# Kernel optimization log

Hardware: AMD Instinct MI355X
Metric: run time of the kernel (lower is better)

## Reference

```python
import jax, jax.numpy as jnp
import numpy as np

B, N, D = 8, 2048, 512  # batch, input_dim (tokens), weight_dim


def setup_inputs() -> dict:
    key = jax.random.key(0)
    ks = jax.random.split(key, 7)
    return {
        "query": jax.random.normal(ks[0], (B, N, D), dtype=jnp.float32),
        "key": jax.random.normal(ks[1], (B, N, D), dtype=jnp.float32),
        "value": jax.random.normal(ks[2], (B, N, D), dtype=jnp.float32),
        "W_query": jax.random.normal(ks[3], (D, D), dtype=jnp.float32),
        "W_key": jax.random.normal(ks[4], (D, D), dtype=jnp.float32),
        "W_value": jax.random.normal(ks[5], (D, D), dtype=jnp.float32),
        "self_importance": jnp.zeros((N,), dtype=jnp.float32),
    }


def reference(query, key, value, W_query, W_key, W_value, self_importance):
    d = W_query.shape[0]
    q = jnp.einsum("bnd,de->bne", query, W_query)
    k = jnp.einsum("bnd,de->bne", key, W_key)
    v = jnp.einsum("bnd,de->bne", value, W_value)
    scores = jnp.einsum("bqe,bke->bqk", q, k) / jnp.sqrt(jnp.float32(d))
    # diagonal self-importance bias: eye(N) * clamp(exp(s), max=3)
    importance = jnp.minimum(jnp.exp(self_importance), 3.0)  # [N]
    n = scores.shape[1]
    idx = jnp.arange(n)
    scores = scores.at[:, idx, idx].add(importance)
    attn = jax.nn.softmax(scores, axis=-1)  # [B, N, N]
    entropy_loss = -jnp.mean(jnp.sum(attn * jnp.log(attn + 1e-10), axis=-1))
    out = jnp.einsum("bqk,bke->bqe", attn, v)
    return (out, attn, entropy_loss)
```

## Files before the change

### kernel.cpp

```cpp
#include <hip/hip_runtime.h>
#include <math.h>

#define BB 8
#define NN 2048
#define DD 512

typedef _Float16 half8 __attribute__((ext_vector_type(8)));
typedef _Float16 half4 __attribute__((ext_vector_type(4)));
typedef float f32x4 __attribute__((ext_vector_type(4)));

#define GLOAD16(gp, sp) __builtin_amdgcn_global_load_lds( \
    (const __attribute__((address_space(1))) void*)(gp), \
    (__attribute__((address_space(3))) void*)(sp), 16, 0, 0)

__global__ __launch_bounds__(256) void wsplit_kernel(
    const float* __restrict__ Wq, const float* __restrict__ Wk, const float* __restrict__ Wv,
    _Float16* __restrict__ qhT, _Float16* __restrict__ qlT,
    _Float16* __restrict__ khT, _Float16* __restrict__ klT,
    _Float16* __restrict__ vhT)
{
    __shared__ float t[64][65];
    const int z = blockIdx.z;
    const float* W = (z == 0) ? Wq : ((z == 1) ? Wk : Wv);
    _Float16* Ph = (z == 0) ? qhT : ((z == 1) ? khT : vhT);
    _Float16* Pl = (z == 0) ? qlT : ((z == 1) ? klT : nullptr);
    const int bx = blockIdx.x * 64, by = blockIdx.y * 64;
    const int tid = threadIdx.x;
    #pragma unroll
    for (int i = 0; i < 16; ++i) {
        const int idx = i * 256 + tid;
        const int r = idx >> 6, c = idx & 63;
        t[r][c] = W[(long)(by + r) * 512 + bx + c];
    }
    __syncthreads();
    #pragma unroll
    for (int i = 0; i < 16; ++i) {
        const int idx = i * 256 + tid;
        const int r = idx >> 6, c = idx & 63;
        const float v = t[c][r];
        const _Float16 h = (_Float16)v;
        const long o = (long)(bx + r) * 512 + by + c;
        Ph[o] = h;
        if (z < 2) Pl[o] = (_Float16)(v - (float)h);
    }
}

template<int EPI>
__global__ __launch_bounds__(256) void mm_nt(
    const float* __restrict__ Af,
    const _Float16* __restrict__ Agh, const _Float16* __restrict__ Agl,
    const _Float16* __restrict__ Bgh, const _Float16* __restrict__ Bgl,
    float* __restrict__ Of, _Float16* __restrict__ Oh, _Float16* __restrict__ Ol,
    const float* __restrict__ si,
    int N, int K, long sAb, long sBb, long sOb, float scale)
{
    constexpr bool NP3    = (EPI == 0 || EPI == 2);
    constexpr bool A_FP32 = (EPI == 0 || EPI == 1);
    constexpr bool A_SPLIT = (EPI == 0);

    __shared__ __align__(16) _Float16 smem[(NP3 ? 4 : 2) * 128 * 32];
    _Float16* Ah = smem;
    _Float16* Bh = smem + 4096;
    _Float16* Al = smem + 8192;
    _Float16* Bl = smem + 12288;

    const int tid  = threadIdx.x;
    const int lane = tid & 63;
    const int w    = tid >> 6;
    const int wr   = w >> 1, wc = w & 1;
    const int z    = blockIdx.z;
    const int bm   = blockIdx.y * 128, bn = blockIdx.x * 128;

    const float* Afz = nullptr;
    const _Float16 *Aghz = nullptr, *Aglz = nullptr;
    if constexpr (A_FP32) { Afz = Af + (long)z * sAb; }
    else { Aghz = Agh + (long)z * sAb; if constexpr (NP3) Aglz = Agl + (long)z * sAb; }
    const _Float16* Bghz = Bgh + (long)z * sBb;
    const _Float16* Bglz = nullptr;
    if constexpr (NP3) Bglz = Bgl + (long)z * sBb;

    f32x4 acc[4][4];
    #pragma unroll
    for (int i = 0; i < 4; ++i)
        #pragma unroll
        for (int j = 0; j < 4; ++j) acc[i][j] = (f32x4)0.0f;

    for (int k0 = 0; k0 < K; k0 += 32) {
        #pragma unroll
        for (int i = 0; i < 2; ++i) {
            const int c   = i * 256 + w * 64 + lane;
            const int row = c >> 2, sl = c & 3;
            const long g  = (long)(bn + row) * K + k0 + sl * 8;
            const int lb  = (i * 256 + w * 64) * 8;
            GLOAD16(Bghz + g, Bh + lb);
            if constexpr (NP3) GLOAD16(Bglz + g, Bl + lb);
        }
        if constexpr (A_FP32) {
            #pragma unroll
            for (int i = 0; i < 4; ++i) {
                const int c = tid + i * 256;
                const int row = c >> 3, q4 = c & 7;
                const float4 v = *(const float4*)(Afz + (long)(bm + row) * K + k0 + q4 * 4);
                half4 h;
                h[0] = (_Float16)v.x; h[1] = (_Float16)v.y;
                h[2] = (_Float16)v.z; h[3] = (_Float16)v.w;
                *(half4*)&Ah[row * 32 + q4 * 4] = h;
                if constexpr (A_SPLIT) {
                    half4 l;
                    l[0] = (_Float16)(v.x - (float)h[0]);
                    l[1] = (_Float16)(v.y - (float)h[1]);
                    l[2] = (_Float16)(v.z - (float)h[2]);
                    l[3] = (_Float16)(v.w - (float)h[3]);
                    *(half4*)&Al[row * 32 + q4 * 4] = l;
                }
            }
        } else {
            #pragma unroll
            for (int i = 0; i < 2; ++i) {
                const int c   = i * 256 + w * 64 + lane;
                const int row = c >> 2, sl = c & 3;
                const long g  = (long)(bm + row) * K + k0 + sl * 8;
                const int lb  = (i * 256 + w * 64) * 8;
                GLOAD16(Aghz + g, Ah + lb);
                if constexpr (NP3) GLOAD16(Aglz + g, Al + lb);
            }
        }
        __syncthreads();

        half8 ah[4], bh[4], al[4], bl[4];
        #pragma unroll
        for (int f = 0; f < 4; ++f) {
            const int ar = wr * 64 + f * 16 + (lane & 15);
            const int ao = ar * 32 + ((lane >> 4) << 3);
            ah[f] = *(const half8*)&Ah[ao];
            if constexpr (NP3) al[f] = *(const half8*)&Al[ao];
            const int br = wc * 64 + f * 16 + (lane & 15);
            const int bo = br * 32 + ((lane >> 4) << 3);
            bh[f] = *(const half8*)&Bh[bo];
            if constexpr (NP3) bl[f] = *(const half8*)&Bl[bo];
        }
        #pragma unroll
        for (int i = 0; i < 4; ++i)
            #pragma unroll
            for (int j = 0; j < 4; ++j) {
                acc[i][j] = __builtin_amdgcn_mfma_f32_16x16x32_f16(ah[i], bh[j], acc[i][j], 0, 0, 0);
                if constexpr (NP3) {
                    acc[i][j] = __builtin_amdgcn_mfma_f32_16x16x32_f16(ah[i], bl[j], acc[i][j], 0, 0, 0);
                    acc[i][j] = __builtin_amdgcn_mfma_f32_16x16x32_f16(al[i], bh[j], acc[i][j], 0, 0, 0);
                }
            }
        __syncthreads();
    }

    #pragma unroll
    for (int i = 0; i < 4; ++i) {
        const int rb = bm + wr * 64 + i * 16 + ((lane >> 4) << 2);
        #pragma unroll
        for (int j = 0; j < 4; ++j) {
            const int gc = bn + wc * 64 + j * 16 + (lane & 15);
            if constexpr (EPI == 0) {
                #pragma unroll
                for (int r = 0; r < 4; ++r) {
                    const float vv = acc[i][j][r];
                    const _Float16 h = (_Float16)vv;
                    const long o = (long)(rb + r) * N + gc;
                    Oh[o] = h;
                    Ol[o] = (_Float16)(vv - (float)h);
                }
            } else if constexpr (EPI == 1) {
                half4 hv;
                #pragma unroll
                for (int r = 0; r < 4; ++r) hv[r] = (_Float16)acc[i][j][r];
                const int b = rb >> 11, rIn = rb & 2047;
                *(half4*)&Oh[((long)b * 512 + gc) * 2048 + rIn] = hv;
            } else if constexpr (EPI == 2) {
                float* O = Of + (long)z * sOb;
                #pragma unroll
                for (int r = 0; r < 4; ++r) {
                    const int gr = rb + r;
                    float vv = acc[i][j][r] * scale;
                    if (gr == gc) vv += fminf(expf(si[gr]), 3.0f);
                    O[(long)gr * N + gc] = vv;
                }
            } else {
                float* O = Of + (long)z * sOb;
                #pragma unroll
                for (int r = 0; r < 4; ++r)
                    O[(long)(rb + r) * N + gc] = acc[i][j][r];
            }
        }
    }
}

__global__ __launch_bounds__(256) void softmax_entropy_kernel(
    float* __restrict__ attn, _Float16* __restrict__ ah, float* __restrict__ partials)
{
    __shared__ float red[4];
    const long row = blockIdx.x;
    float* p = attn + row * (long)NN;
    _Float16* ph = ah + row * (long)NN;
    const int tid = threadIdx.x;
    const int base = tid * 8;

    float4 va = *(const float4*)(p + base);
    float4 vb = *(const float4*)(p + base + 4);
    float v[8] = {va.x, va.y, va.z, va.w, vb.x, vb.y, vb.z, vb.w};

    float m = v[0];
    #pragma unroll
    for (int i = 1; i < 8; ++i) m = fmaxf(m, v[i]);
    #pragma unroll
    for (int o = 32; o; o >>= 1) m = fmaxf(m, __shfl_xor(m, o, 64));
    if ((tid & 63) == 0) red[tid >> 6] = m;
    __syncthreads();
    m = fmaxf(fmaxf(red[0], red[1]), fmaxf(red[2], red[3]));

    float t[8];
    float s = 0.f;
    #pragma unroll
    for (int i = 0; i < 8; ++i) { t[i] = v[i] - m; v[i] = expf(t[i]); s += v[i]; }
    #pragma unroll
    for (int o = 32; o; o >>= 1) s += __shfl_xor(s, o, 64);
    __syncthreads();
    if ((tid & 63) == 0) red[tid >> 6] = s;
    __syncthreads();
    s = red[0] + red[1] + red[2] + red[3];

    const float inv = 1.0f / s;
    const float lns = logf(s);
    float e = 0.f;
    float pv[8];
    #pragma unroll
    for (int i = 0; i < 8; ++i) {
        pv[i] = v[i] * inv;
        e = fmaf(pv[i], t[i] - lns, e);
    }
    *(float4*)(p + base)     = make_float4(pv[0], pv[1], pv[2], pv[3]);
    *(float4*)(p + base + 4) = make_float4(pv[4], pv[5], pv[6], pv[7]);
    half8 h;
    #pragma unroll
    for (int i = 0; i < 8; ++i) h[i] = (_Float16)pv[i];
    *(half8*)(ph + base) = h;

    #pragma unroll
    for (int o = 32; o; o >>= 1) e += __shfl_xor(e, o, 64);
    __syncthreads();
    if ((tid & 63) == 0) red[tid >> 6] = e;
    __syncthreads();
    if (tid == 0) partials[row] = red[0] + red[1] + red[2] + red[3];
}

__global__ __launch_bounds__(256) void ent_reduce_kernel(
    const float* __restrict__ partials, float* __restrict__ ent)
{
    __shared__ float red[4];
    float s = 0.f;
    for (int i = threadIdx.x; i < BB * NN; i += 256) s += partials[i];
    #pragma unroll
    for (int o = 32; o; o >>= 1) s += __shfl_xor(s, o, 64);
    if ((threadIdx.x & 63) == 0) red[threadIdx.x >> 6] = s;
    __syncthreads();
    if (threadIdx.x == 0)
        *ent = -(red[0] + red[1] + red[2] + red[3]) / (float)(BB * NN);
}

extern "C" void kernel_launch(void* const* d_in, const int* in_sizes, int n_in,
                              void* d_out, int out_size, void* d_ws, size_t ws_size,
                              hipStream_t stream) {
    const float* query = (const float*)d_in[0];
    const float* key   = (const float*)d_in[1];
    const float* value = (const float*)d_in[2];
    const float* Wq    = (const float*)d_in[3];
    const float* Wk    = (const float*)d_in[4];
    const float* Wv    = (const float*)d_in[5];
    const float* si    = (const float*)d_in[6];

    float* out  = (float*)d_out;
    float* attn = out + (size_t)BB * NN * DD;
    float* ent  = attn + (size_t)BB * NN * NN;

    const size_t NK = (size_t)BB * NN * DD;
    _Float16* ws16 = (_Float16*)d_ws;
    _Float16* qh = ws16;
    _Float16* ql = qh + NK;
    _Float16* kh = ql + NK;
    _Float16* kl = kh + NK;
    _Float16* vT = kl + NK;
    _Float16* WqhT = vT + NK;
    _Float16* WqlT = WqhT + DD * DD;
    _Float16* WkhT = WqlT + DD * DD;
    _Float16* WklT = WkhT + DD * DD;
    _Float16* WvhT = WklT + DD * DD;
    float* partials = (float*)(WvhT + DD * DD);
    _Float16* attn_h = ws16;

    const dim3 blk(256);
    const float inv_sqrt_d = 0.044194173824159216f;

    wsplit_kernel<<<dim3(8, 8, 3), blk, 0, stream>>>(Wq, Wk, Wv,
        WqhT, WqlT, WkhT, WklT, WvhT);

    mm_nt<0><<<dim3(4, 128, 1), blk, 0, stream>>>(
        query, nullptr, nullptr, WqhT, WqlT, nullptr, qh, ql, nullptr,
        DD, DD, 0, 0, 0, 1.0f);
    mm_nt<0><<<dim3(4, 128, 1), blk, 0, stream>>>(
        key, nullptr, nullptr, WkhT, WklT, nullptr, kh, kl, nullptr,
        DD, DD, 0, 0, 0, 1.0f);
    mm_nt<1><<<dim3(4, 128, 1), blk, 0, stream>>>(
        value, nullptr, nullptr, WvhT, nullptr, nullptr, vT, nullptr, nullptr,
        DD, DD, 0, 0, 0, 1.0f);

    mm_nt<2><<<dim3(16, 16, BB), blk, 0, stream>>>(
        nullptr, qh, ql, kh, kl, attn, nullptr, nullptr, si,
        NN, DD, (long)NN * DD, (long)NN * DD, (long)NN * NN, inv_sqrt_d);

    softmax_entropy_kernel<<<dim3(BB * NN), blk, 0, stream>>>(attn, attn_h, partials);
    ent_reduce_kernel<<<dim3(1), blk, 0, stream>>>(partials, ent);

    mm_nt<3><<<dim3(4, 16, BB), blk, 0, stream>>>(
        nullptr, attn_h, nullptr, vT, nullptr, out, nullptr, nullptr, nullptr,
        DD, NN, (long)NN * NN, (long)DD * NN, (long)NN * DD, 1.0f);
}
```

Baseline: 348.5 us.

## Replace scores GEMM with 256x256-tile double-buffered split-fp16 MFMA kernel

The QK^T scores GEMM moves from the generic 128x128 mm_nt kernel to a dedicated 512-thread kernel with 256x256 output tiles. It uses a register-staged double-buffered LDS pipeline with an XOR swizzle, MFMA priority hints, and a remapped block order for L2 locality. The goal is more data reuse per tile and overlap of global loads with MFMA work in the three-product hi/lo fp16 compensation GEMM. The cost is 128KB of dynamic LDS and a large accumulator footprint per thread, which limits occupancy and risks register spills.

```diff
diff --git a/kernel.cpp b/kernel.cpp
--- a/kernel.cpp
+++ b/kernel.cpp
@@ -5,6 +5,7 @@
 #define NN 2048
 #define DD 512
 
+typedef _Float16 halfT;
 typedef _Float16 half8 __attribute__((ext_vector_type(8)));
 typedef _Float16 half4 __attribute__((ext_vector_type(4)));
 typedef float f32x4 __attribute__((ext_vector_type(4)));
@@ -54,7 +55,7 @@
     const float* __restrict__ si,
     int N, int K, long sAb, long sBb, long sOb, float scale)
 {
-    constexpr bool NP3    = (EPI == 0 || EPI == 2);
+    constexpr bool NP3    = (EPI == 0);
     constexpr bool A_FP32 = (EPI == 0 || EPI == 1);
     constexpr bool A_SPLIT = (EPI == 0);
 
@@ -122,7 +123,6 @@
                 const long g  = (long)(bm + row) * K + k0 + sl * 8;
                 const int lb  = (i * 256 + w * 64) * 8;
                 GLOAD16(Aghz + g, Ah + lb);
-                if constexpr (NP3) GLOAD16(Aglz + g, Al + lb);
             }
         }
         __syncthreads();
@@ -173,20 +173,151 @@
                 for (int r = 0; r < 4; ++r) hv[r] = (_Float16)acc[i][j][r];
                 const int b = rb >> 11, rIn = rb & 2047;
                 *(half4*)&Oh[((long)b * 512 + gc) * 2048 + rIn] = hv;
-            } else if constexpr (EPI == 2) {
-                float* O = Of + (long)z * sOb;
-                #pragma unroll
-                for (int r = 0; r < 4; ++r) {
-                    const int gr = rb + r;
-                    float vv = acc[i][j][r] * scale;
-                    if (gr == gc) vv += fminf(expf(si[gr]), 3.0f);
-                    O[(long)gr * N + gc] = vv;
-                }
             } else {
                 float* O = Of + (long)z * sOb;
                 #pragma unroll
                 for (int r = 0; r < 4; ++r)
                     O[(long)(rb + r) * N + gc] = acc[i][j][r];
+            }
+        }
+    }
+}
+
+__global__ __launch_bounds__(512, 2) void scores256_kernel(
+    const halfT* __restrict__ qh, const halfT* __restrict__ ql,
+    const halfT* __restrict__ kh, const halfT* __restrict__ kl,
+    float* __restrict__ C, const float* __restrict__ si, float scale)
+{
+    extern __shared__ __align__(16) char smem[];
+
+    const int tid  = threadIdx.x;
+    const int lane = tid & 63;
+    const int w    = tid >> 6;
+    const int wr   = w >> 2, wc = w & 3;
+
+    int flat = (blockIdx.z << 6) | (blockIdx.y << 3) | blockIdx.x;
+    flat = ((flat & 7) << 6) | (flat >> 3);
+    const int bx = flat & 7, by = (flat >> 3) & 7, bz = flat >> 6;
+    const int bm = by * 256, bn = bx * 256;
+
+    const long zoff = (long)bz * NN * DD;
+    const halfT* A_h = qh + zoff;
+    const halfT* A_l = ql + zoff;
+    const halfT* B_h = kh + zoff;
+    const halfT* B_l = kl + zoff;
+
+    const int s_row0 = tid >> 2, s_sl = tid & 3;
+    const int s_row1 = s_row0 + 128;
+    const int s_off0 = s_row0 * 64 + ((s_sl ^ (s_row0 & 3)) << 4);
+    const int s_off1 = s_row1 * 64 + ((s_sl ^ (s_row1 & 3)) << 4);
+    const long gA0 = (long)(bm + s_row0) * DD + s_sl * 8;
+    const long gA1 = (long)(bm + s_row1) * DD + s_sl * 8;
+    const long gB0 = (long)(bn + s_row0) * DD + s_sl * 8;
+    const long gB1 = (long)(bn + s_row1) * DD + s_sl * 8;
+
+    const int q = lane >> 4;
+    const int frag_off = (lane & 15) * 64 + ((q ^ (lane & 3)) << 4);
+    const int aoff = wr * 8192 + frag_off;
+    const int boff = wc * 4096 + frag_off;
+
+    f32x4 acc[8][4];
+    #pragma unroll
+    for (int m = 0; m < 8; ++m)
+        #pragma unroll
+        for (int n = 0; n < 4; ++n) acc[m][n] = (f32x4)0.0f;
+
+    float4 sreg[8];
+    auto load_tile = [&](int t) {
+        const long kk = (long)t * 32;
+        sreg[0] = *(const float4*)(A_h + gA0 + kk);
+        sreg[1] = *(const float4*)(A_h + gA1 + kk);
+        sreg[2] = *(const float4*)(A_l + gA0 + kk);
+        sreg[3] = *(const float4*)(A_l + gA1 + kk);
+        sreg[4] = *(const float4*)(B_h + gB0 + kk);
+        sreg[5] = *(const float4*)(B_h + gB1 + kk);
+        sreg[6] = *(const float4*)(B_l + gB0 + kk);
+        sreg[7] = *(const float4*)(B_l + gB1 + kk);
+    };
+    auto write_tile = [&](char* setp) {
+        *(float4*)(setp +     0 + s_off0) = sreg[0];
+        *(float4*)(setp +     0 + s_off1) = sreg[1];
+        *(float4*)(setp + 16384 + s_off0) = sreg[2];
+        *(float4*)(setp + 16384 + s_off1) = sreg[3];
+        *(float4*)(setp + 32768 + s_off0) = sreg[4];
+        *(float4*)(setp + 32768 + s_off1) = sreg[5];
+        *(float4*)(setp + 49152 + s_off0) = sreg[6];
+        *(float4*)(setp + 49152 + s_off1) = sreg[7];
+    };
+
+    load_tile(0);
+    write_tile(smem);
+    load_tile(1);
+    asm volatile("s_waitcnt lgkmcnt(0)" ::: "memory");
+    __builtin_amdgcn_s_barrier();
+    __builtin_amdgcn_sched_barrier(0);
+
+    for (int t = 0; t < 16; ++t) {
+        char* cur = smem + (size_t)(t & 1) * 65536;
+        char* nxt = smem + (size_t)((t + 1) & 1) * 65536;
+
+        if (t < 15) write_tile(nxt);
+        if (t < 14) load_tile(t + 2);
+        __builtin_amdgcn_sched_barrier(0);
+
+        half8 ah[8], bh[4], bl[4];
+        #pragma unroll
+        for (int n = 0; n < 4; ++n)
+            bh[n] = *(const half8*)(cur + 32768 + boff + n * 1024);
+        #pragma unroll
+        for (int m = 0; m < 8; ++m)
+            ah[m] = *(const half8*)(cur +     0 + aoff + m * 1024);
+        __builtin_amdgcn_s_setprio(1);
+        #pragma unroll
+        for (int m = 0; m < 8; ++m)
+            #pragma unroll
+            for (int n = 0; n < 4; ++n)
+                acc[m][n] = __builtin_amdgcn_mfma_f32_16x16x32_f16(ah[m], bh[n], acc[m][n], 0, 0, 0);
+        __builtin_amdgcn_s_setprio(0);
+        #pragma unroll
+        for (int n = 0; n < 4; ++n)
+            bl[n] = *(const half8*)(cur + 49152 + boff + n * 1024);
+        __builtin_amdgcn_s_setprio(1);
+        #pragma unroll
+        for (int m = 0; m < 8; ++m)
+            #pragma unroll
+            for (int n = 0; n < 4; ++n)
+                acc[m][n] = __builtin_amdgcn_mfma_f32_16x16x32_f16(ah[m], bl[n], acc[m][n], 0, 0, 0);
+        __builtin_amdgcn_s_setprio(0);
+        __builtin_amdgcn_s_setprio(1);
+        #pragma unroll
+        for (int m = 0; m < 8; ++m) {
+            const half8 al = *(const half8*)(cur + 16384 + aoff + m * 1024);
+            #pragma unroll
+            for (int n = 0; n < 4; ++n)
+                acc[m][n] = __builtin_amdgcn_mfma_f32_16x16x32_f16(al, bh[n], acc[m][n], 0, 0, 0);
+        }
+        __builtin_amdgcn_s_setprio(0);
+
+        if (t < 15) {
+            asm volatile("s_waitcnt lgkmcnt(0)" ::: "memory");
+            __builtin_amdgcn_s_barrier();
+            __builtin_amdgcn_sched_barrier(0);
+        }
+    }
+
+    float* Cz = C + (long)bz * NN * NN;
+    #pragma unroll
+    for (int m = 0; m < 8; ++m) {
+        const int rb = bm + wr * 128 + m * 16 + ((lane >> 4) << 2);
+        #pragma unroll
+        for (int n = 0; n < 4; ++n) {
+            const int gc = bn + wc * 64 + n * 16 + (lane & 15);
+            #pragma unroll
+            for (int r = 0; r < 4; ++r) {
+                const int gr = rb + r;
+                float vv = acc[m][n][r] * scale;
+                if (gr == gc) vv += fminf(expf(si[gr]), 3.0f);
+                Cz[(long)gr * NN + gc] = vv;
             }
         }
     }
@@ -310,9 +441,8 @@
         value, nullptr, nullptr, WvhT, nullptr, nullptr, vT, nullptr, nullptr,
         DD, DD, 0, 0, 0, 1.0f);
 
-    mm_nt<2><<<dim3(16, 16, BB), blk, 0, stream>>>(
-        nullptr, qh, ql, kh, kl, attn, nullptr, nullptr, si,
-        NN, DD, (long)NN * DD, (long)NN * DD, (long)NN * NN, inv_sqrt_d);
+    scores256_kernel<<<dim3(8, 8, 8), dim3(512), 131072, stream>>>(
+        qh, ql, kh, kl, attn, si, inv_sqrt_d);
 
     softmax_entropy_kernel<<<dim3(BB * NN), blk, 0, stream>>>(attn, attn_h, partials);
     ent_reduce_kernel<<<dim3(1), blk, 0, stream>>>(partials, ent);
```

After: 450.0 us. +29.1%, slower.
